# Kernel tuning notes

Hardware: AMD Instinct MI355X
Metric: run time of the kernel (lower is better)

## Reference

```python
import jax, jax.numpy as jnp
import numpy as np
import math

B, S, DIM, H = 2, 2048, 1024, 16
DH = DIM // H          # 64, per-head dim
DFF = 2048             # FCLayer hidden
NEG = -1.0e9


def setup_inputs() -> dict:
    key = jax.random.key(0)
    ks = jax.random.split(key, 10)
    glorot = jax.nn.initializers.glorot_uniform()
    de_x = jax.random.normal(ks[0], (B, S, DIM), dtype=jnp.float32)
    en_x = jax.random.normal(ks[1], (B, S, DIM), dtype=jnp.float32)
    # causal mask: 1.0 where attention is disallowed (upper triangle)
    mask = jnp.triu(jnp.ones((S, S), dtype=jnp.float32), k=1)
    # Stacked per-head projection weights for the (shared) attn_heads.
    Wq = glorot(ks[2], (H, DIM, DH), jnp.float32)
    Wk = glorot(ks[3], (H, DIM, DH), jnp.float32)
    Wv = glorot(ks[4], (H, DIM, DH), jnp.float32)
    W1 = glorot(ks[5], (DIM, DFF), jnp.float32)
    b1 = jnp.zeros((DFF,), jnp.float32)
    W2 = glorot(ks[6], (DFF, DIM), jnp.float32)
    b2 = jnp.zeros((DIM,), jnp.float32)
    return {"de_x": de_x, "en_x": en_x, "mask": mask,
            "Wq": Wq, "Wk": Wk, "Wv": Wv,
            "W1": W1, "b1": b1, "W2": W2, "b2": b2}


def _multihead(q_x, k_x, v_x, Wq, Wk, Wv, mask):
    # q_x/k_x/v_x: [B,S,DIM]; W*: [H,DIM,DH]
    q = jnp.einsum('bsd,hde->bhse', q_x, Wq)
    k = jnp.einsum('bsd,hde->bhse', k_x, Wk)
    v = jnp.einsum('bsd,hde->bhse', v_x, Wv)
    p = jnp.einsum('bhse,bhte->bhst', q, k) / math.sqrt(DH)
    if mask is not None:
        p = p + mask * NEG
    p = jax.nn.softmax(p, axis=-1)
    h = jnp.einsum('bhst,bhte->bhse', p, v)      # [B,H,S,DH]
    # concat heads along feature dim -> [B,S,DIM]
    return h.transpose(0, 2, 1, 3).reshape(q_x.shape[0], q_x.shape[1], -1)


def reference(de_x, en_x, mask, Wq, Wk, Wv, W1, b1, W2, b2):
    # Faithful to the source: compute_multihead_output ignores its attn_heads
    # arg and always uses self.attn_heads, and binds head(q=outer_en, k=outer_en,
    # v=outer_de). So:
    #   h1 = MHA(q=de_x, k=de_x, v=de_x, mask) with attn_heads weights
    #   h2 = MHA(q=en_x, k=en_x, v=h1, None)   with the SAME weights
    h1 = _multihead(de_x, de_x, de_x, Wq, Wk, Wv, mask)
    h2 = _multihead(en_x, en_x, h1, Wq, Wk, Wv, None)
    ff1 = jax.nn.relu(h2 @ W1 + b1)
    y = ff1 @ W2 + b2
    return y
```

## Files before the change

kernel.cpp:

```cpp
#include <hip/hip_runtime.h>
#include <stdint.h>


#define DEV static __device__ __forceinline__

typedef __attribute__((ext_vector_type(8))) __bf16 bf16x8;
typedef __attribute__((ext_vector_type(8))) unsigned short u16x8;
typedef __attribute__((ext_vector_type(4))) float f32x4;

DEV float bf2f(uint16_t u) { union { uint32_t u; float f; } v; v.u = ((uint32_t)u) << 16; return v.f; }
DEV uint16_t f2bf(float f) {
  union { float f; uint32_t u; } v; v.f = f;
  uint32_t r = v.u + 0x7fffu + ((v.u >> 16) & 1u);
  return (uint16_t)(r >> 16);
}
DEV uint16_t f2bf_hw(float f) { return __builtin_bit_cast(unsigned short, (__bf16)f); }

DEV bf16x8 asbf(u16x8 v) { return __builtin_bit_cast(bf16x8, v); }
DEV f32x4 mfma32(bf16x8 a, bf16x8 b, f32x4 c) {
  return __builtin_amdgcn_mfma_f32_16x16x32_bf16(a, b, c, 0, 0, 0);
}

DEV int swz(int row, int slot) { return slot ^ (row & 7); }

DEV bf16x8 frag8(const uint16_t* l, int row, int slot) {
  u16x8 v = *(const u16x8*)((const char*)l + row * 128 + (swz(row, slot) << 4));
  return asbf(v);
}

__global__ void probe_k(const uint32_t* __restrict__ mask, uint32_t* __restrict__ flag) {
  flag[0] = (mask[1] & 0xFFFFu) ? 1u : 0u;
}

__global__ __launch_bounds__(256) void cvt_k(const void* __restrict__ src,
                                             uint16_t* __restrict__ dst, int n,
                                             const uint32_t* __restrict__ flag) {
  const int isbf = (int)flag[0];
  const int stride = gridDim.x * 256 * 8;
  for (int i = (blockIdx.x * 256 + threadIdx.x) * 8; i < n; i += stride) {
    if (isbf) {
      *(u16x8*)(dst + i) = *(const u16x8*)((const uint16_t*)src + i);
    } else {
      const float* sf = (const float*)src + i;
      u16x8 o;
      for (int j = 0; j < 8; j++) o[j] = f2bf(sf[j]);
      *(u16x8*)(dst + i) = o;
    }
  }
}

__global__ __launch_bounds__(256) void transpose_k(const void* __restrict__ in_,
                                                   uint16_t* __restrict__ out, int R, int C,
                                                   float scale,
                                                   const uint32_t* __restrict__ flag) {
  __shared__ uint16_t t[32][33];
  const int isbf = (int)flag[0];
  const int b = blockIdx.z;
  const float* in_f = (const float*)in_ + (size_t)b * R * C;
  const uint16_t* in_u = (const uint16_t*)in_ + (size_t)b * R * C;
  out += (size_t)b * R * C;
  const int c0 = blockIdx.x * 32, r0 = blockIdx.y * 32;
  const int tx = threadIdx.x & 31, ty = threadIdx.x >> 5;
  for (int i = 0; i < 4; i++) {
    int r = ty + i * 8;
    size_t idx = (size_t)(r0 + r) * C + c0 + tx;
    uint16_t v;
    if (isbf) v = (scale == 1.0f) ? in_u[idx] : f2bf(bf2f(in_u[idx]) * scale);
    else      v = f2bf(in_f[idx] * scale);
    t[r][tx] = v;
  }
  __syncthreads();
  for (int i = 0; i < 4; i++) {
    int r = ty + i * 8;
    out[(size_t)(c0 + r) * R + r0 + tx] = t[tx][r];
  }
}

__global__ __launch_bounds__(256) void proj_k(
    const uint16_t* __restrict__ A_qk, const uint16_t* __restrict__ A_v,
    const uint16_t* __restrict__ Wtq, const uint16_t* __restrict__ Wtk,
    const uint16_t* __restrict__ Wtv,
    uint16_t* __restrict__ Q, uint16_t* __restrict__ K, uint16_t* __restrict__ Vt) {
  __shared__ __attribute__((aligned(16))) uint16_t lA[2][128 * 64];
  __shared__ __attribute__((aligned(16))) uint16_t lB[2][64 * 64];
  const int tid = threadIdx.x, lane = tid & 63, wave = tid >> 6;
  const int g = lane >> 4;
  const int m0 = blockIdx.x * 128;
  const int h = blockIdx.y & 15, proj = blockIdx.y >> 4;
  const int b = blockIdx.z;
  const uint16_t* A = (proj == 2 ? A_v : A_qk) + (size_t)b * 2048 * 1024;
  const uint16_t* Bt = (proj == 0 ? Wtq : proj == 1 ? Wtk : Wtv) + (size_t)h * 64 * 1024;
  const int wm = wave >> 1, wn = wave & 1;
  f32x4 acc[4][2] = {};
  u16x8 ra[4], rb[2];
  const int rowA0 = tid >> 3, slotA = tid & 7;
  auto loadT = [&](int kt) {
    for (int i = 0; i < 4; i++)
      ra[i] = *(const u16x8*)(A + (size_t)(m0 + rowA0 + i * 32) * 1024 + kt + slotA * 8);
    for (int i = 0; i < 2; i++)
      rb[i] = *(const u16x8*)(Bt + (size_t)(rowA0 + i * 32) * 1024 + kt + slotA * 8);
  };
  auto writeT = [&](int buf) {
    for (int i = 0; i < 4; i++) {
      int row = rowA0 + i * 32;
      *(u16x8*)&lA[buf][(row * 8 + swz(row, slotA)) * 8] = ra[i];
    }
    for (int i = 0; i < 2; i++) {
      int row = rowA0 + i * 32;
      *(u16x8*)&lB[buf][(row * 8 + swz(row, slotA)) * 8] = rb[i];
    }
  };
  loadT(0);
  writeT(0);
  int cur = 0;
  for (int it = 0; it < 16; it++) {
    const int more = (it < 15);
    if (more) loadT((it + 1) * 64);
    __syncthreads();
    for (int kk = 0; kk < 2; kk++) {
      bf16x8 af[4], bfr[2];
      for (int fm = 0; fm < 4; fm++) af[fm] = frag8(lA[cur], wm * 64 + fm * 16 + (lane & 15), kk * 4 + g);
      for (int fn = 0; fn < 2; fn++) bfr[fn] = frag8(lB[cur], wn * 32 + fn * 16 + (lane & 15), kk * 4 + g);
      for (int fm = 0; fm < 4; fm++)
        for (int fn = 0; fn < 2; fn++)
          acc[fm][fn] = mfma32(af[fm], bfr[fn], acc[fm][fn]);
    }
    if (more) writeT(cur ^ 1);
    cur ^= 1;
  }
  const size_t bh = (size_t)(b * 16 + h);
  if (proj != 2) {
    uint16_t* outp = (proj == 0 ? Q : K);
    for (int fm = 0; fm < 4; fm++)
      for (int fn = 0; fn < 2; fn++)
        for (int r = 0; r < 4; r++) {
          int s = m0 + wm * 64 + fm * 16 + g * 4 + r;
          int e = wn * 32 + fn * 16 + (lane & 15);
          outp[(bh * 2048 + s) * 64 + e] = f2bf(acc[fm][fn][r]);
        }
  } else {
    __syncthreads();
    uint16_t* tv = lA[0];
    for (int fm = 0; fm < 4; fm++)
      for (int fn = 0; fn < 2; fn++)
        for (int r = 0; r < 4; r++) {
          int s = wm * 64 + fm * 16 + g * 4 + r;
          int e = wn * 32 + fn * 16 + (lane & 15);
          tv[e * 128 + s] = f2bf(acc[fm][fn][r]);
        }
    __syncthreads();
    for (int e = tid >> 4; e < 64; e += 16) {
      int s = (tid & 15) * 8;
      *(u16x8*)(Vt + (bh * 64 + e) * 2048 + m0 + s) = *(const u16x8*)&tv[e * 128 + s];
    }
  }
}

template <int CAUSAL>
__global__ __launch_bounds__(256) void attn_k(const uint16_t* __restrict__ Q,
                                              const uint16_t* __restrict__ K,
                                              const uint16_t* __restrict__ Vt,
                                              uint16_t* __restrict__ O) {
  __shared__ __attribute__((aligned(16))) uint16_t lK[64 * 64];
  __shared__ __attribute__((aligned(16))) uint16_t lV[64 * 64];
  __shared__ __attribute__((aligned(16))) uint16_t lP[4][16 * 64];
  const int tid = threadIdx.x, lane = tid & 63, wave = tid >> 6;
  const int g = lane >> 4;
  const int h = blockIdx.y, b = blockIdx.z;
  const size_t bh = (size_t)(b * 16 + h);
  const uint16_t* Qg = Q + bh * 2048 * 64;
  const uint16_t* Kg = K + bh * 2048 * 64;
  const uint16_t* Vg = Vt + bh * 64 * 2048;
  uint16_t* lPw = lP[wave];
  bf16x8 ones;
  for (int j = 0; j < 8; j++) ones[j] = (__bf16)1.0f;
  uint32_t pbase[4];
  for (int r = 0; r < 4; r++) {
    int row = g * 4 + r;
    pbase[r] = row * 128 + (((((lane & 15) >> 3)) ^ (row & 7)) << 4) + ((lane & 7) << 1);
  }
  u16x8 rk[2], rv[2];
  const int row0 = tid >> 3, slot0 = tid & 7;
  auto loadKV = [&](int kt) {
    for (int i = 0; i < 2; i++) {
      int row = row0 + i * 32;
      rk[i] = *(const u16x8*)(Kg + (size_t)(kt * 64 + row) * 64 + slot0 * 8);
      rv[i] = *(const u16x8*)(Vg + (size_t)row * 2048 + kt * 64 + slot0 * 8);
    }
  };
  auto writeKV = [&]() {
    for (int i = 0; i < 2; i++) {
      int row = row0 + i * 32;
      *(u16x8*)&lK[(row * 8 + swz(row, slot0)) * 8] = rk[i];
      *(u16x8*)&lV[(row * 8 + swz(row, slot0)) * 8] = rv[i];
    }
  };
  const int npass = CAUSAL ? 2 : 1;
  for (int pass = 0; pass < npass; pass++) {
    const int qt = CAUSAL ? (pass ? 31 - (int)blockIdx.x : (int)blockIdx.x) : (int)blockIdx.x;
    const int q0 = qt * 64;
    bf16x8 qf[2];
    {
      int row = q0 + wave * 16 + (lane & 15);
      for (int kk = 0; kk < 2; kk++)
        qf[kk] = asbf(*(const u16x8*)(Qg + (size_t)row * 64 + kk * 32 + g * 8));
    }
    f32x4 oacc[4] = {};
    f32x4 acc_l = {};
    float m_run[4];
    for (int r = 0; r < 4; r++) m_run[r] = -INFINITY;
    const int ktmax = CAUSAL ? qt : 31;
    loadKV(0);
    for (int kt = 0; kt <= ktmax; kt++) {
      const int more = (kt < ktmax);
      __syncthreads();
      writeKV();
      __syncthreads();
      if (more) loadKV(kt + 1);
      f32x4 s[4] = {};
      for (int kk = 0; kk < 2; kk++)
        for (int nf = 0; nf < 4; nf++)
          s[nf] = mfma32(qf[kk], frag8(lK, nf * 16 + (lane & 15), kk * 4 + g), s[nf]);
      if (CAUSAL && kt == qt) {
        for (int nf = 0; nf < 4; nf++)
          for (int r = 0; r < 4; r++) {
            int qloc = wave * 16 + g * 4 + r;
            int kloc = nf * 16 + (lane & 15);
            if (kloc > qloc) s[nf][r] = -1e9f;
          }
      }
      float rloc[4];
      for (int r = 0; r < 4; r++)
        rloc[r] = fmaxf(fmaxf(s[0][r], s[1][r]), fmaxf(s[2][r], s[3][r]));
      bool ok = true;
      for (int r = 0; r < 4; r++) ok = ok && (rloc[r] <= m_run[r] + 8.0f);
      if (!__all(ok)) {
        float rmax[4];
        for (int r = 0; r < 4; r++) rmax[r] = rloc[r];
        for (int m = 1; m < 16; m <<= 1)
          for (int r = 0; r < 4; r++) rmax[r] = fmaxf(rmax[r], __shfl_xor(rmax[r], m));
        for (int r = 0; r < 4; r++) {
          float mn = fmaxf(m_run[r], rmax[r]);
          float alpha = __builtin_amdgcn_exp2f(m_run[r] - mn);
          m_run[r] = mn;
          acc_l[r] *= alpha;
          for (int df = 0; df < 4; df++) oacc[df][r] *= alpha;
        }
      }
      for (int nf = 0; nf < 4; nf++)
        for (int r = 0; r < 4; r++) {
          float p = __builtin_amdgcn_exp2f(s[nf][r] - m_run[r]);
          *(uint16_t*)((char*)lPw + (pbase[r] ^ (nf << 5))) = f2bf_hw(p);
        }
      for (int kk = 0; kk < 2; kk++) {
        bf16x8 pa = frag8(lPw, lane & 15, kk * 4 + g);
        acc_l = mfma32(pa, ones, acc_l);
        for (int df = 0; df < 4; df++)
          oacc[df] = mfma32(pa, frag8(lV, df * 16 + (lane & 15), kk * 4 + g), oacc[df]);
      }
    }
    float inv[4];
    for (int r = 0; r < 4; r++) inv[r] = 1.0f / acc_l[r];
    for (int df = 0; df < 4; df++)
      for (int r = 0; r < 4; r++) {
        int srow = q0 + wave * 16 + g * 4 + r;
        int e = df * 16 + (lane & 15);
        O[((size_t)b * 2048 + srow) * 1024 + h * 64 + e] = f2bf(oacc[df][r] * inv[r]);
      }
  }
}

template <int RELU>
__global__ __launch_bounds__(256) void ff_k(const uint16_t* __restrict__ A,
                                            const uint16_t* __restrict__ Bt,
                                            const uint16_t* __restrict__ bias,
                                            uint16_t* __restrict__ C, int Kdim, int N) {
  __shared__ __attribute__((aligned(16))) uint16_t lA[2][128 * 64];
  __shared__ __attribute__((aligned(16))) uint16_t lB[2][128 * 64];
  const int tid = threadIdx.x, lane = tid & 63, wave = tid >> 6;
  const int g = lane >> 4;
  const int m0 = blockIdx.x * 128, n0 = blockIdx.y * 128;
  const int wm = wave >> 1, wn = wave & 1;
  f32x4 acc[4][4] = {};
  u16x8 ra[4], rb[4];
  const int row0 = tid >> 3, slot0 = tid & 7;
  auto loadT = [&](int kt) {
    for (int i = 0; i < 4; i++) {
      int row = row0 + i * 32;
      ra[i] = *(const u16x8*)(A + (size_t)(m0 + row) * Kdim + kt + slot0 * 8);
      rb[i] = *(const u16x8*)(Bt + (size_t)(n0 + row) * Kdim + kt + slot0 * 8);
    }
  };
  auto writeT = [&](int buf) {
    for (int i = 0; i < 4; i++) {
      int row = row0 + i * 32;
      *(u16x8*)&lA[buf][(row * 8 + swz(row, slot0)) * 8] = ra[i];
      *(u16x8*)&lB[buf][(row * 8 + swz(row, slot0)) * 8] = rb[i];
    }
  };
  loadT(0);
  writeT(0);
  int cur = 0;
  const int nit = Kdim >> 6;
  for (int it = 0; it < nit; it++) {
    const int more = (it < nit - 1);
    if (more) loadT((it + 1) * 64);
    __syncthreads();
    for (int kk = 0; kk < 2; kk++) {
      bf16x8 af[4], bfr[4];
      for (int fm = 0; fm < 4; fm++) af[fm] = frag8(lA[cur], wm * 64 + fm * 16 + (lane & 15), kk * 4 + g);
      for (int fn = 0; fn < 4; fn++) bfr[fn] = frag8(lB[cur], wn * 64 + fn * 16 + (lane & 15), kk * 4 + g);
      for (int fm = 0; fm < 4; fm++)
        for (int fn = 0; fn < 4; fn++)
          acc[fm][fn] = mfma32(af[fm], bfr[fn], acc[fm][fn]);
    }
    if (more) writeT(cur ^ 1);
    cur ^= 1;
  }
  for (int fm = 0; fm < 4; fm++)
    for (int fn = 0; fn < 4; fn++) {
      int col = n0 + wn * 64 + fn * 16 + (lane & 15);
      float bv = bf2f(bias[col]);
      for (int r = 0; r < 4; r++) {
        int row = m0 + wm * 64 + fm * 16 + g * 4 + r;
        float v = acc[fm][fn][r] + bv;
        if (RELU) v = fmaxf(v, 0.f);
        C[(size_t)row * N + col] = f2bf(v);
      }
    }
}

__global__ __launch_bounds__(256) void store_k(const uint16_t* __restrict__ yb,
                                               void* __restrict__ out, int n,
                                               const uint32_t* __restrict__ flag) {
  const int isbf = (int)flag[0];
  const int stride = gridDim.x * 256 * 8;
  for (int i = (blockIdx.x * 256 + threadIdx.x) * 8; i < n; i += stride) {
    u16x8 v = *(const u16x8*)(yb + i);
    if (isbf) {
      *(u16x8*)((uint16_t*)out + i) = v;
    } else {
      float* of = (float*)out + i;
      for (int j = 0; j < 8; j++) of[j] = bf2f(v[j]);
    }
  }
}

extern "C" void kernel_launch(void* const* d_in, const int* in_sizes, int n_in,
                              void* d_out, int out_size, void* d_ws, size_t ws_size,
                              hipStream_t stream) {
  const void* de_x = d_in[0];
  const void* en_x = d_in[1];
  const void* mask = d_in[2];
  const void* Wq = d_in[3];
  const void* Wk = d_in[4];
  const void* Wv = d_in[5];
  const void* W1 = d_in[6];
  const void* b1 = d_in[7];
  const void* W2 = d_in[8];
  const void* b2 = d_in[9];

  uint16_t* ws = (uint16_t*)d_ws;
  const size_t M1 = (size_t)1 << 20;
  uint32_t* flag = (uint32_t*)ws;
  uint16_t* b1c = ws + 1024;
  uint16_t* b2c = ws + 4096;
  uint16_t* Wtq = ws + 1 * M1;
  uint16_t* Wtk = ws + 2 * M1;
  uint16_t* Wtv = ws + 3 * M1;
  uint16_t* W1t = ws + 4 * M1;
  uint16_t* W2t = ws + 6 * M1;
  uint16_t* de_c = ws + 8 * M1;
  uint16_t* en_c = ws + 12 * M1;
  uint16_t* Qb  = ws + 16 * M1;
  uint16_t* Kb  = ws + 20 * M1;
  uint16_t* Vtb = ws + 24 * M1;
  uint16_t* h1  = ws + 28 * M1;
  uint16_t* h2  = ws + 32 * M1;
  uint16_t* ff1 = Qb;
  uint16_t* yb  = Vtb;

  const int NX = 2 * 2048 * 1024;
  dim3 blk(256);

  probe_k<<<1, 1, 0, stream>>>((const uint32_t*)mask, flag);
  cvt_k<<<2048, blk, 0, stream>>>(de_x, de_c, NX, flag);
  cvt_k<<<2048, blk, 0, stream>>>(en_x, en_c, NX, flag);
  cvt_k<<<1, blk, 0, stream>>>(b1, b1c, 2048, flag);
  cvt_k<<<1, blk, 0, stream>>>(b2, b2c, 1024, flag);
  transpose_k<<<dim3(2, 32, 16), blk, 0, stream>>>(Wq, Wtq, 1024, 64, 0.180336880f, flag);
  transpose_k<<<dim3(2, 32, 16), blk, 0, stream>>>(Wk, Wtk, 1024, 64, 1.0f, flag);
  transpose_k<<<dim3(2, 32, 16), blk, 0, stream>>>(Wv, Wtv, 1024, 64, 1.0f, flag);
  transpose_k<<<dim3(64, 32, 1), blk, 0, stream>>>(W1, W1t, 1024, 2048, 1.0f, flag);
  transpose_k<<<dim3(32, 64, 1), blk, 0, stream>>>(W2, W2t, 2048, 1024, 1.0f, flag);
  proj_k<<<dim3(16, 48, 2), blk, 0, stream>>>(de_c, de_c, Wtq, Wtk, Wtv, Qb, Kb, Vtb);
  attn_k<1><<<dim3(16, 16, 2), blk, 0, stream>>>(Qb, Kb, Vtb, h1);
  proj_k<<<dim3(16, 48, 2), blk, 0, stream>>>(en_c, h1, Wtq, Wtk, Wtv, Qb, Kb, Vtb);
  attn_k<0><<<dim3(32, 16, 2), blk, 0, stream>>>(Qb, Kb, Vtb, h2);
  ff_k<1><<<dim3(32, 16), blk, 0, stream>>>(h2, W1t, b1c, ff1, 1024, 2048);
  ff_k<0><<<dim3(32, 8), blk, 0, stream>>>(ff1, W2t, b2c, yb, 2048, 1024);
  store_k<<<2048, blk, 0, stream>>>(yb, d_out, out_size, flag);
}
```

Baseline: 283.7 us.

## Split attention over key range with partial softmax merge kernel

Replaces the two-pass causal pairing and one-block-per-query-tile layout with a split-K (flash-decoding style) scheme. Long causal query tiles and all non-causal tiles are split into two key-range halves, each writing unnormalized bf16 partial outputs plus running max and sum. A new merge kernel combines the partials. This raises the block count to fill more CUs (only 512 and 1024 blocks before), at the cost of extra global traffic, an extra launch, and bf16 rounding of the unnormalized partials.

```diff
diff --git a/kernel.cpp b/kernel.cpp
--- a/kernel.cpp
+++ b/kernel.cpp
@@ -160,13 +160,30 @@
 __global__ __launch_bounds__(256) void attn_k(const uint16_t* __restrict__ Q,
                                               const uint16_t* __restrict__ K,
                                               const uint16_t* __restrict__ Vt,
-                                              uint16_t* __restrict__ O) {
+                                              uint16_t* __restrict__ Op0,
+                                              uint16_t* __restrict__ Op1,
+                                              float* __restrict__ mbuf,
+                                              float* __restrict__ lbuf) {
   __shared__ __attribute__((aligned(16))) uint16_t lK[64 * 64];
   __shared__ __attribute__((aligned(16))) uint16_t lV[64 * 64];
   __shared__ __attribute__((aligned(16))) uint16_t lP[4][16 * 64];
   const int tid = threadIdx.x, lane = tid & 63, wave = tid >> 6;
   const int g = lane >> 4;
-  const int h = blockIdx.y, b = blockIdx.z;
+  const int bx = blockIdx.x, h = blockIdx.y, b = blockIdx.z;
+  int qt, split, kt0, kt1;
+  if (CAUSAL) {
+    if (bx < 32) {
+      qt = 31 - (bx >> 1);
+      split = bx & 1;
+      int n0 = (qt + 1) >> 1;
+      kt0 = split ? n0 : 0;
+      kt1 = split ? (qt + 1) : n0;
+    } else {
+      qt = 47 - bx; split = 0; kt0 = 0; kt1 = qt + 1;
+    }
+  } else {
+    qt = bx & 31; split = bx >> 5; kt0 = split * 16; kt1 = kt0 + 16;
+  }
   const size_t bh = (size_t)(b * 16 + h);
   const uint16_t* Qg = Q + bh * 2048 * 64;
   const uint16_t* Kg = K + bh * 2048 * 64;
@@ -195,79 +212,113 @@
       *(u16x8*)&lV[(row * 8 + swz(row, slot0)) * 8] = rv[i];
     }
   };
-  const int npass = CAUSAL ? 2 : 1;
-  for (int pass = 0; pass < npass; pass++) {
-    const int qt = CAUSAL ? (pass ? 31 - (int)blockIdx.x : (int)blockIdx.x) : (int)blockIdx.x;
-    const int q0 = qt * 64;
-    bf16x8 qf[2];
-    {
-      int row = q0 + wave * 16 + (lane & 15);
-      for (int kk = 0; kk < 2; kk++)
-        qf[kk] = asbf(*(const u16x8*)(Qg + (size_t)row * 64 + kk * 32 + g * 8));
-    }
-    f32x4 oacc[4] = {};
-    f32x4 acc_l = {};
-    float m_run[4];
-    for (int r = 0; r < 4; r++) m_run[r] = -INFINITY;
-    const int ktmax = CAUSAL ? qt : 31;
-    loadKV(0);
-    for (int kt = 0; kt <= ktmax; kt++) {
-      const int more = (kt < ktmax);
-      __syncthreads();
-      writeKV();
-      __syncthreads();
-      if (more) loadKV(kt + 1);
-      f32x4 s[4] = {};
-      for (int kk = 0; kk < 2; kk++)
-        for (int nf = 0; nf < 4; nf++)
-          s[nf] = mfma32(qf[kk], frag8(lK, nf * 16 + (lane & 15), kk * 4 + g), s[nf]);
-      if (CAUSAL && kt == qt) {
-        for (int nf = 0; nf < 4; nf++)
-          for (int r = 0; r < 4; r++) {
-            int qloc = wave * 16 + g * 4 + r;
-            int kloc = nf * 16 + (lane & 15);
-            if (kloc > qloc) s[nf][r] = -1e9f;
-          }
-      }
-      float rloc[4];
-      for (int r = 0; r < 4; r++)
-        rloc[r] = fmaxf(fmaxf(s[0][r], s[1][r]), fmaxf(s[2][r], s[3][r]));
-      bool ok = true;
-      for (int r = 0; r < 4; r++) ok = ok && (rloc[r] <= m_run[r] + 8.0f);
-      if (!__all(ok)) {
-        float rmax[4];
-        for (int r = 0; r < 4; r++) rmax[r] = rloc[r];
-        for (int m = 1; m < 16; m <<= 1)
-          for (int r = 0; r < 4; r++) rmax[r] = fmaxf(rmax[r], __shfl_xor(rmax[r], m));
-        for (int r = 0; r < 4; r++) {
-          float mn = fmaxf(m_run[r], rmax[r]);
-          float alpha = __builtin_amdgcn_exp2f(m_run[r] - mn);
-          m_run[r] = mn;
-          acc_l[r] *= alpha;
-          for (int df = 0; df < 4; df++) oacc[df][r] *= alpha;
-        }
-      }
+  const int q0 = qt * 64;
+  bf16x8 qf[2];
+  {
+    int row = q0 + wave * 16 + (lane & 15);
+    for (int kk = 0; kk < 2; kk++)
+      qf[kk] = asbf(*(const u16x8*)(Qg + (size_t)row * 64 + kk * 32 + g * 8));
+  }
+  f32x4 oacc[4] = {};
+  f32x4 acc_l = {};
+  float m_run[4];
+  for (int r = 0; r < 4; r++) m_run[r] = -INFINITY;
+  loadKV(kt0);
+  for (int kt = kt0; kt < kt1; kt++) {
+    const int more = (kt < kt1 - 1);
+    __syncthreads();
+    writeKV();
+    __syncthreads();
+    if (more) loadKV(kt + 1);
+    f32x4 s[4] = {};
+    for (int kk = 0; kk < 2; kk++)
+      for (int nf = 0; nf < 4; nf++)
+        s[nf] = mfma32(qf[kk], frag8(lK, nf * 16 + (lane & 15), kk * 4 + g), s[nf]);
+    if (CAUSAL && kt == qt) {
       for (int nf = 0; nf < 4; nf++)
         for (int r = 0; r < 4; r++) {
-          float p = __builtin_amdgcn_exp2f(s[nf][r] - m_run[r]);
-          *(uint16_t*)((char*)lPw + (pbase[r] ^ (nf << 5))) = f2bf_hw(p);
+          int qloc = wave * 16 + g * 4 + r;
+          int kloc = nf * 16 + (lane & 15);
+          if (kloc > qloc) s[nf][r] = -1e9f;
         }
-      for (int kk = 0; kk < 2; kk++) {
-        bf16x8 pa = frag8(lPw, lane & 15, kk * 4 + g);
-        acc_l = mfma32(pa, ones, acc_l);
-        for (int df = 0; df < 4; df++)
-          oacc[df] = mfma32(pa, frag8(lV, df * 16 + (lane & 15), kk * 4 + g), oacc[df]);
+    }
+    float rloc[4];
+    for (int r = 0; r < 4; r++)
+      rloc[r] = fmaxf(fmaxf(s[0][r], s[1][r]), fmaxf(s[2][r], s[3][r]));
+    bool ok = true;
+    for (int r = 0; r < 4; r++) ok = ok && (rloc[r] <= m_run[r] + 8.0f);
+    if (!__all(ok)) {
+      float rmax[4];
+      for (int r = 0; r < 4; r++) rmax[r] = rloc[r];
+      for (int m = 1; m < 16; m <<= 1)
+        for (int r = 0; r < 4; r++) rmax[r] = fmaxf(rmax[r], __shfl_xor(rmax[r], m));
+      for (int r = 0; r < 4; r++) {
+        float mn = fmaxf(m_run[r], rmax[r]);
+        float alpha = __builtin_amdgcn_exp2f(m_run[r] - mn);
+        m_run[r] = mn;
+        acc_l[r] *= alpha;
+        for (int df = 0; df < 4; df++) oacc[df][r] *= alpha;
       }
     }
-    float inv[4];
-    for (int r = 0; r < 4; r++) inv[r] = 1.0f / acc_l[r];
-    for (int df = 0; df < 4; df++)
+    for (int nf = 0; nf < 4; nf++)
       for (int r = 0; r < 4; r++) {
-        int srow = q0 + wave * 16 + g * 4 + r;
-        int e = df * 16 + (lane & 15);
-        O[((size_t)b * 2048 + srow) * 1024 + h * 64 + e] = f2bf(oacc[df][r] * inv[r]);
+        float p = __builtin_amdgcn_exp2f(s[nf][r] - m_run[r]);
+        *(uint16_t*)((char*)lPw + (pbase[r] ^ (nf << 5))) = f2bf_hw(p);
       }
-  }
+    for (int kk = 0; kk < 2; kk++) {
+      bf16x8 pa = frag8(lPw, lane & 15, kk * 4 + g);
+      acc_l = mfma32(pa, ones, acc_l);
+      for (int df = 0; df < 4; df++)
+        oacc[df] = mfma32(pa, frag8(lV, df * 16 + (lane & 15), kk * 4 + g), oacc[df]);
+    }
+  }
+  uint16_t* Op = split ? Op1 : Op0;
+  for (int df = 0; df < 4; df++)
+    for (int r = 0; r < 4; r++) {
+      int srow = q0 + wave * 16 + g * 4 + r;
+      int e = df * 16 + (lane & 15);
+      Op[((size_t)b * 2048 + srow) * 1024 + h * 64 + e] = f2bf(oacc[df][r]);
+    }
+  if ((lane & 15) == 0) {
+    for (int r = 0; r < 4; r++) {
+      int srow = q0 + wave * 16 + g * 4 + r;
+      size_t idx = ((size_t)(split * 2 + b) * 16 + h) * 2048 + srow;
+      mbuf[idx] = m_run[r];
+      lbuf[idx] = acc_l[r];
+    }
+  }
+}
+
+template <int CAUSAL>
+__global__ __launch_bounds__(256) void merge_k(const uint16_t* __restrict__ O0,
+                                               const uint16_t* __restrict__ O1,
+                                               const float* __restrict__ mbuf,
+                                               const float* __restrict__ lbuf,
+                                               uint16_t* __restrict__ out) {
+  int i = (blockIdx.x * 256 + threadIdx.x) * 8;
+  int sg = i >> 10;
+  int b = sg >> 11, s = sg & 2047;
+  int h = (i & 1023) >> 6;
+  size_t i0 = ((size_t)b * 16 + h) * 2048 + s;
+  size_t i1 = ((size_t)(2 + b) * 16 + h) * 2048 + s;
+  float m0 = mbuf[i0], l0 = lbuf[i0];
+  u16x8 o0 = *(const u16x8*)(O0 + i);
+  bool two = CAUSAL ? ((s >> 6) >= 16) : true;
+  u16x8 o;
+  if (two) {
+    float m1 = mbuf[i1], l1 = lbuf[i1];
+    float M = fmaxf(m0, m1);
+    float a0 = __builtin_amdgcn_exp2f(m0 - M);
+    float a1 = __builtin_amdgcn_exp2f(m1 - M);
+    float inv = 1.f / (a0 * l0 + a1 * l1);
+    u16x8 o1v = *(const u16x8*)(O1 + i);
+    for (int j = 0; j < 8; j++)
+      o[j] = f2bf((a0 * bf2f(o0[j]) + a1 * bf2f(o1v[j])) * inv);
+  } else {
+    float inv = 1.f / l0;
+    for (int j = 0; j < 8; j++) o[j] = f2bf(bf2f(o0[j]) * inv);
+  }
+  *(u16x8*)(out + i) = o;
 }
 
 template <int RELU>
@@ -365,6 +416,8 @@
   uint32_t* flag = (uint32_t*)ws;
   uint16_t* b1c = ws + 1024;
   uint16_t* b2c = ws + 4096;
+  float* mbuf = (float*)(ws + 8192);
+  float* lbuf = (float*)(ws + 8192 + 262144);
   uint16_t* Wtq = ws + 1 * M1;
   uint16_t* Wtk = ws + 2 * M1;
   uint16_t* Wtv = ws + 3 * M1;
@@ -379,6 +432,9 @@
   uint16_t* h2  = ws + 32 * M1;
   uint16_t* ff1 = Qb;
   uint16_t* yb  = Vtb;
+  uint16_t* Op0 = de_c;
+  uint16_t* Op1a = h2;
+  uint16_t* Op1b = h1;
 
   const int NX = 2 * 2048 * 1024;
   dim3 blk(256);
@@ -394,9 +450,11 @@
   transpose_k<<<dim3(64, 32, 1), blk, 0, stream>>>(W1, W1t, 1024, 2048, 1.0f, flag);
   transpose_k<<<dim3(32, 64, 1), blk, 0, stream>>>(W2, W2t, 2048, 1024, 1.0f, flag);
   proj_k<<<dim3(16, 48, 2), blk, 0, stream>>>(de_c, de_c, Wtq, Wtk, Wtv, Qb, Kb, Vtb);
-  attn_k<1><<<dim3(16, 16, 2), blk, 0, stream>>>(Qb, Kb, Vtb, h1);
+  attn_k<1><<<dim3(48, 16, 2), blk, 0, stream>>>(Qb, Kb, Vtb, Op0, Op1a, mbuf, lbuf);
+  merge_k<1><<<2048, blk, 0, stream>>>(Op0, Op1a, mbuf, lbuf, h1);
   proj_k<<<dim3(16, 48, 2), blk, 0, stream>>>(en_c, h1, Wtq, Wtk, Wtv, Qb, Kb, Vtb);
-  attn_k<0><<<dim3(32, 16, 2), blk, 0, stream>>>(Qb, Kb, Vtb, h2);
+  attn_k<0><<<dim3(64, 16, 2), blk, 0, stream>>>(Qb, Kb, Vtb, Op0, Op1b, mbuf, lbuf);
+  merge_k<0><<<2048, blk, 0, stream>>>(Op0, Op1b, mbuf, lbuf, h2);
   ff_k<1><<<dim3(32, 16), blk, 0, stream>>>(h2, W1t, b1c, ff1, 1024, 2048);
   ff_k<0><<<dim3(32, 8), blk, 0, stream>>>(ff1, W2t, b2c, yb, 2048, 1024);
   store_k<<<2048, blk, 0, stream>>>(yb, d_out, out_size, flag);
```

Measured after the change: 294.4 us. +3.8%, slower.
